# Performance work log

Hardware: AMD Instinct MI355X
Metric: run time of the kernel (lower is better)

## Reference

```python
import jax, jax.numpy as jnp
import numpy as np

DIM = 128
HEADS = 4
WIN = 7
N = WIN * WIN  # 49 tokens per window
B = 64         # images
BDIM = 64      # windows per image (56/7)^2
B_ = B * BDIM  # 4096 total windows
HEAD_DIM = DIM // HEADS
SCALE = HEAD_DIM ** (-0.5)


def _rel_index():
    ch, cw = np.meshgrid(np.arange(WIN), np.arange(WIN), indexing='ij')
    coords = np.stack([ch.ravel(), cw.ravel()])            # [2, N]
    rel = coords[:, :, None] - coords[:, None, :]          # [2, N, N]
    rel = rel.transpose(1, 2, 0).astype(np.int32)
    rel[:, :, 0] += WIN - 1
    rel[:, :, 1] += WIN - 1
    rel[:, :, 0] *= 2 * WIN - 1
    return jnp.asarray(rel.sum(-1))                        # [N, N] in [0, 169)


def setup_inputs() -> dict:
    key = jax.random.key(0)
    ks = jax.random.split(key, 7)
    return {
        'x': jax.random.normal(ks[0], (B_, N, DIM), jnp.float32),
        'q_global': jax.random.normal(ks[1], (B, 1, HEADS, N, HEAD_DIM), jnp.float32),
        'rel_bias_table': jax.random.normal(ks[2], (169, HEADS), jnp.float32) * 0.02,
        'W_kv': jax.random.normal(ks[3], (DIM, 2 * DIM), jnp.float32) / np.sqrt(DIM),
        'b_kv': jnp.zeros((2 * DIM,), jnp.float32),
        'W_proj': jax.random.normal(ks[4], (DIM, DIM), jnp.float32) / np.sqrt(DIM),
        'b_proj': jnp.zeros((DIM,), jnp.float32),
        'rel_index': _rel_index(),
    }


def reference(x, q_global, rel_bias_table, W_kv, b_kv, W_proj, b_proj, rel_index):
    Bw, n, C = x.shape
    Bg = q_global.shape[0]
    bdim = Bw // Bg
    # kv projection: [B_, N, 2, H, hd] -> k, v each [B_, H, N, hd]
    kv = (x @ W_kv + b_kv).reshape(Bw, n, 2, HEADS, HEAD_DIM)
    kv = kv.transpose(2, 0, 3, 1, 4)
    k, v = kv[0], kv[1]
    # broadcast global q over windows of each image
    q = jnp.broadcast_to(q_global, (Bg, bdim, HEADS, n, HEAD_DIM)).reshape(Bw, HEADS, n, HEAD_DIM)
    attn = jnp.einsum('bhnd,bhmd->bhnm', q * SCALE, k)
    bias = rel_bias_table[rel_index]                        # [N, N, H]
    attn = attn + bias.transpose(2, 0, 1)[None]
    attn = jax.nn.softmax(attn, axis=-1)
    out = jnp.einsum('bhnm,bhmd->bhnd', attn, v)
    out = out.transpose(0, 2, 1, 3).reshape(Bw, n, C)
    return out @ W_proj + b_proj
```

## Files before the change

kernel.cpp:

```cpp
#include <hip/hip_runtime.h>

#define SCALE 0.17677669529663687f

typedef __attribute__((ext_vector_type(8))) short bf16x8;
typedef __attribute__((ext_vector_type(4))) short bf16x4;
typedef __attribute__((ext_vector_type(4))) float f32x4;

__device__ inline short cvt_bf16(float f) {
    union { float f; unsigned u; } v; v.f = f;
    unsigned r = v.u + 0x7fffu + ((v.u >> 16) & 1u);
    return (short)(r >> 16);
}
__device__ inline short cvt_bf16_fast(float f) {
    union { float f; unsigned u; } v; v.f = f;
    return (short)((v.u + 0x8000u) >> 16);
}
__device__ inline unsigned pack_bf16x2(float f0, float f1) {
    union { float f; unsigned u; } a, b; a.f = f0; b.f = f1;
    return __builtin_amdgcn_perm(b.u + 0x8000u, a.u + 0x8000u, 0x07060302u);
}

#if __has_builtin(__builtin_amdgcn_mfma_f32_16x16x16bf16_1k)
__device__ inline f32x4 mfma16x16(bf16x4 a, bf16x4 b, f32x4 c) {
    return __builtin_amdgcn_mfma_f32_16x16x16bf16_1k(a, b, c, 0, 0, 0);
}
#else
__device__ inline f32x4 mfma16x16(bf16x4 a, bf16x4 b, f32x4 c) {
    asm("v_mfma_f32_16x16x16_bf16 %0, %1, %2, %0" : "+v"(c) : "v"(a), "v"(b));
    return c;
}
#endif

#define WS_WPT  32768
#define WS_QW   49152
#define WS_BIAS 450560

__global__ void prep_kernel(const float* __restrict__ qg,
                            const float* __restrict__ rbt,
                            const float* __restrict__ wkv,
                            const float* __restrict__ wpj,
                            const int*   __restrict__ ridx,
                            short* __restrict__ ws) {
    int i = blockIdx.x * 256 + threadIdx.x;
    if (i < 32768) {
        int c = i >> 7, k = i & 127;
        ws[i] = cvt_bf16(wkv[k * 256 + c]);
        return;
    }
    i -= 32768;
    if (i < 16384) {
        int c = i >> 7, k = i & 127;
        ws[WS_WPT + i] = cvt_bf16(wpj[k * 128 + c]);
        return;
    }
    i -= 16384;
    if (i < 100352) {
        float4 q4 = *(const float4*)(qg + (long)i * 4);
        unsigned lo = (unsigned)(unsigned short)cvt_bf16(q4.x * SCALE) |
                      ((unsigned)(unsigned short)cvt_bf16(q4.y * SCALE) << 16);
        unsigned hi = (unsigned)(unsigned short)cvt_bf16(q4.z * SCALE) |
                      ((unsigned)(unsigned short)cvt_bf16(q4.w * SCALE) << 16);
        uint2 u; u.x = lo; u.y = hi;
        *(uint2*)(ws + WS_QW + (long)i * 4) = u;
        return;
    }
    i -= 100352;
    if (i < 12544) {
        int h = i / 3136, rem = i % 3136, ir = rem >> 6, j = rem & 63;
        float* bias = (float*)(ws + WS_BIAS);
        bias[i] = (j < 49) ? rbt[ridx[ir * 49 + j] * 4 + h] : 0.f;
    }
}

#define KOFF    6664
#define KSLOT   1960
#define SMEM_SZ 14504

__global__ __launch_bounds__(256, 4) void win_attn_kernel(
        const float* __restrict__ x,
        const short* __restrict__ ws,
        const float* __restrict__ bkv,
        const float* __restrict__ bpj,
        float* __restrict__ out) {
    const int b    = blockIdx.x;
    const int img  = b >> 6;
    const int tid  = threadIdx.x;
    const int w    = tid >> 6;
    const int lane = tid & 63;
    const int quad = lane >> 4;
    const int l16  = lane & 15;

    const short* wkvt  = ws;
    const short* wpt   = ws + WS_WPT;
    const short* qw    = ws + WS_QW;
    const float* biasb = (const float*)(ws + WS_BIAS);

    __shared__ __align__(16) short smem[SMEM_SZ];
    short* xs = smem;
    short* os = smem;

    const f32x4 fzero = {0.f, 0.f, 0.f, 0.f};
    const int h = w;

    const float* xb = x + (long)b * 49 * 128;
    #pragma unroll
    for (int it = 0; it < 4; ++it) {
        int chunk = tid + it * 256;
        if (chunk < 784) {
            int row = chunk >> 4, c8 = (chunk & 15) * 8;
            const float* p = xb + row * 128 + c8;
            float4 a = *(const float4*)p;
            float4 c = *(const float4*)(p + 4);
            union { uint4 u; bf16x8 v; } pk;
            pk.u.x = pack_bf16x2(a.x, a.y);
            pk.u.y = pack_bf16x2(a.z, a.w);
            pk.u.z = pack_bf16x2(c.x, c.y);
            pk.u.w = pack_bf16x2(c.z, c.w);
            *(bf16x8*)(xs + row * 136 + c8) = pk.v;
        }
    }
    __syncthreads();

    short* ksl = smem + KOFF + h * KSLOT;
    {
        f32x4 acck[2][4];
        #pragma unroll
        for (int nt = 0; nt < 2; ++nt)
            #pragma unroll
            for (int mi = 0; mi < 4; ++mi) acck[nt][mi] = fzero;

        #pragma unroll
        for (int kk = 0; kk < 4; ++kk) {
            bf16x8 bfr[2];
            #pragma unroll
            for (int nt = 0; nt < 2; ++nt)
                bfr[nt] = *(const bf16x8*)(wkvt + (h * 32 + nt * 16 + l16) * 128 + kk * 32 + quad * 8);
            #pragma unroll
            for (int mi = 0; mi < 4; ++mi) {
                int tok = mi * 16 + l16; if (tok > 48) tok = 48;
                bf16x8 af = *(const bf16x8*)(xs + tok * 136 + kk * 32 + quad * 8);
                #pragma unroll
                for (int nt = 0; nt < 2; ++nt)
                    acck[nt][mi] = __builtin_amdgcn_mfma_f32_16x16x32_bf16(af, bfr[nt], acck[nt][mi], 0, 0, 0);
            }
        }
        #pragma unroll
        for (int nt = 0; nt < 2; ++nt) {
            const int d = nt * 16 + l16;
            const float bv = bkv[h * 32 + d];
            short* kdst = ksl + d;
            #pragma unroll
            for (int mi = 0; mi < 4; ++mi)
                #pragma unroll
                for (int r = 0; r < 4; ++r) {
                    int tok = mi * 16 + quad * 4 + r;
                    if (tok < 49) kdst[tok * 40] = cvt_bf16_fast(acck[nt][mi][r] + bv);
                }
        }
    }

    bf16x4 vfrag[2][4];
    {
        f32x4 accv[2][4];
        #pragma unroll
        for (int nv = 0; nv < 2; ++nv)
            #pragma unroll
            for (int mi = 0; mi < 4; ++mi) accv[nv][mi] = fzero;

        #pragma unroll
        for (int kk = 0; kk < 4; ++kk) {
            bf16x8 bfr[2];
            #pragma unroll
            for (int nv = 0; nv < 2; ++nv)
                bfr[nv] = *(const bf16x8*)(wkvt + (128 + h * 32 + nv * 16 + l16) * 128 + kk * 32 + quad * 8);
            #pragma unroll
            for (int mi = 0; mi < 4; ++mi) {
                int tok = mi * 16 + l16; if (tok > 48) tok = 48;
                bf16x8 af = *(const bf16x8*)(xs + tok * 136 + kk * 32 + quad * 8);
                #pragma unroll
                for (int nv = 0; nv < 2; ++nv)
                    accv[nv][mi] = __builtin_amdgcn_mfma_f32_16x16x32_bf16(af, bfr[nv], accv[nv][mi], 0, 0, 0);
            }
        }
        #pragma unroll
        for (int nv = 0; nv < 2; ++nv) {
            const float bv = bkv[128 + h * 32 + nv * 16 + l16];
            #pragma unroll
            for (int kt = 0; kt < 4; ++kt) {
                union { unsigned u[2]; bf16x4 v; } pk;
                pk.u[0] = pack_bf16x2(accv[nv][kt][0] + bv, accv[nv][kt][1] + bv);
                pk.u[1] = pack_bf16x2(accv[nv][kt][2] + bv, accv[nv][kt][3] + bv);
                vfrag[nv][kt] = pk.v;
            }
        }
    }

    const short* qh = qw + (long)(img * 4 + h) * 49 * 32;
    f32x4 oacc[4][2];
    #pragma unroll
    for (int mo = 0; mo < 4; ++mo)
        #pragma unroll
        for (int nv = 0; nv < 2; ++nv) oacc[mo][nv] = fzero;

    #pragma unroll
    for (int ni = 0; ni < 4; ++ni) {
        int ic = ni * 16 + l16; if (ic > 48) ic = 48;
        bf16x8 qf = *(const bf16x8*)(qh + ic * 32 + quad * 8);
        f32x4 sacc[4] = {fzero, fzero, fzero, fzero};
        #pragma unroll
        for (int mi = 0; mi < 4; ++mi) {
            int kr = mi * 16 + l16; if (kr > 48) kr = 48;
            bf16x8 kf = *(const bf16x8*)(ksl + kr * 40 + quad * 8);
            sacc[mi] = __builtin_amdgcn_mfma_f32_16x16x32_bf16(kf, qf, sacc[mi], 0, 0, 0);
        }
        const float* bp = biasb + (h * 49 + ic) * 64;
        #pragma unroll
        for (int mi = 0; mi < 4; ++mi) {
            float4 b4 = *(const float4*)(bp + mi * 16 + quad * 4);
            float bb[4] = {b4.x, b4.y, b4.z, b4.w};
            #pragma unroll
            for (int r = 0; r < 4; ++r) {
                int j = mi * 16 + quad * 4 + r;
                sacc[mi][r] = (j < 49) ? (sacc[mi][r] + bb[r]) : -3.0e38f;
            }
        }
        float m = -3.0e38f;
        #pragma unroll
        for (int mi = 0; mi < 4; ++mi)
            #pragma unroll
            for (int r = 0; r < 4; ++r) m = fmaxf(m, sacc[mi][r]);
        m = fmaxf(m, __shfl_xor(m, 16, 64));
        m = fmaxf(m, __shfl_xor(m, 32, 64));
        float sum = 0.f;
        #pragma unroll
        for (int mi = 0; mi < 4; ++mi)
            #pragma unroll
            for (int r = 0; r < 4; ++r) {
                float e = __expf(sacc[mi][r] - m);
                sacc[mi][r] = e; sum += e;
            }
        sum += __shfl_xor(sum, 16, 64);
        sum += __shfl_xor(sum, 32, 64);
        float inv = 1.0f / sum;
        #pragma unroll
        for (int kt = 0; kt < 4; ++kt) {
            union { unsigned u[2]; bf16x4 v; } pk;
            pk.u[0] = pack_bf16x2(sacc[kt][0] * inv, sacc[kt][1] * inv);
            pk.u[1] = pack_bf16x2(sacc[kt][2] * inv, sacc[kt][3] * inv);
            #pragma unroll
            for (int nv = 0; nv < 2; ++nv)
                oacc[ni][nv] = mfma16x16(pk.v, vfrag[nv][kt], oacc[ni][nv]);
        }
    }

    __syncthreads();

    #pragma unroll
    for (int mo = 0; mo < 4; ++mo)
        #pragma unroll
        for (int nv = 0; nv < 2; ++nv)
            #pragma unroll
            for (int r = 0; r < 4; ++r) {
                int tok = mo * 16 + quad * 4 + r;
                os[tok * 136 + h * 32 + nv * 16 + l16] = cvt_bf16_fast(oacc[mo][nv][r]);
            }
    __syncthreads();

    f32x4 pacc[2][4];
    #pragma unroll
    for (int ct = 0; ct < 2; ++ct)
        #pragma unroll
        for (int mi = 0; mi < 4; ++mi) pacc[ct][mi] = fzero;
    #pragma unroll
    for (int kk = 0; kk < 4; ++kk) {
        bf16x8 ofrag[4];
        #pragma unroll
        for (int mi = 0; mi < 4; ++mi)
            ofrag[mi] = *(const bf16x8*)(os + (mi * 16 + l16) * 136 + kk * 32 + quad * 8);
        #pragma unroll
        for (int ct = 0; ct < 2; ++ct) {
            const int c0 = (w * 2 + ct) * 16;
            bf16x8 wfrag = *(const bf16x8*)(wpt + (c0 + l16) * 128 + kk * 32 + quad * 8);
            #pragma unroll
            for (int mi = 0; mi < 4; ++mi)
                pacc[ct][mi] = __builtin_amdgcn_mfma_f32_16x16x32_bf16(ofrag[mi], wfrag, pacc[ct][mi], 0, 0, 0);
        }
    }
    #pragma unroll
    for (int ct = 0; ct < 2; ++ct) {
        const int c0 = (w * 2 + ct) * 16;
        const float bb = bpj[c0 + l16];
        #pragma unroll
        for (int mi = 0; mi < 4; ++mi)
            #pragma unroll
            for (int r = 0; r < 4; ++r) {
                int tok = mi * 16 + quad * 4 + r;
                if (tok < 49)
                    out[((long)b * 49 + tok) * 128 + c0 + l16] = pacc[ct][mi][r] + bb;
            }
    }
}

extern "C" void kernel_launch(void* const* d_in, const int* in_sizes, int n_in,
                              void* d_out, int out_size, void* d_ws, size_t ws_size,
                              hipStream_t stream) {
    const float* x    = (const float*)d_in[0];
    const float* qg   = (const float*)d_in[1];
    const float* rbt  = (const float*)d_in[2];
    const float* wkv  = (const float*)d_in[3];
    const float* bkv  = (const float*)d_in[4];
    const float* wpj  = (const float*)d_in[5];
    const float* bpj  = (const float*)d_in[6];
    const int*   ridx = (const int*)d_in[7];
    short* ws = (short*)d_ws;

    const int prep_total = 32768 + 16384 + 100352 + 12544;
    prep_kernel<<<(prep_total + 255) / 256, 256, 0, stream>>>(qg, rbt, wkv, wpj, ridx, ws);
    win_attn_kernel<<<4096, 256, 0, stream>>>(x, ws, bkv, bpj, (float*)d_out);
}
```

Measured before the change: 270.4 us.

## Load x fragments directly from global into registers, skipping LDS staging

Each wave now loads its x MFMA A-operand fragments straight from global memory into registers, converting to bf16 there, instead of staging the whole tile in LDS and syncing. K slots and the output tile get separate, non-overlapping LDS regions, so one __syncthreads before the output write can be dropped. Output rows are clamped and guarded to 49 tokens. Each of the four waves now reads the full x tile from global (or cache) itself, and the 16 fragment registers held across both projections raise register pressure.

```diff
diff --git a/kernel.cpp b/kernel.cpp
--- a/kernel.cpp
+++ b/kernel.cpp
@@ -72,8 +72,8 @@
     }
 }
 
-#define KOFF    6664
 #define KSLOT   1960
+#define OOFF    7840
 #define SMEM_SZ 14504
 
 __global__ __launch_bounds__(256, 4) void win_attn_kernel(
@@ -96,19 +96,24 @@
     const float* biasb = (const float*)(ws + WS_BIAS);
 
     __shared__ __align__(16) short smem[SMEM_SZ];
-    short* xs = smem;
-    short* os = smem;
+    short* os = smem + OOFF;
 
     const f32x4 fzero = {0.f, 0.f, 0.f, 0.f};
     const int h = w;
 
     const float* xb = x + (long)b * 49 * 128;
-    #pragma unroll
-    for (int it = 0; it < 4; ++it) {
-        int chunk = tid + it * 256;
-        if (chunk < 784) {
-            int row = chunk >> 4, c8 = (chunk & 15) * 8;
-            const float* p = xb + row * 128 + c8;
+    const float* xrow[4];
+    #pragma unroll
+    for (int mi = 0; mi < 4; ++mi) {
+        int tok = mi * 16 + l16; if (tok > 48) tok = 48;
+        xrow[mi] = xb + tok * 128 + quad * 8;
+    }
+    bf16x8 xfrag[4][4];
+    #pragma unroll
+    for (int kk = 0; kk < 4; ++kk)
+        #pragma unroll
+        for (int mi = 0; mi < 4; ++mi) {
+            const float* p = xrow[mi] + kk * 32;
             float4 a = *(const float4*)p;
             float4 c = *(const float4*)(p + 4);
             union { uint4 u; bf16x8 v; } pk;
@@ -116,12 +121,10 @@
             pk.u.y = pack_bf16x2(a.z, a.w);
             pk.u.z = pack_bf16x2(c.x, c.y);
             pk.u.w = pack_bf16x2(c.z, c.w);
-            *(bf16x8*)(xs + row * 136 + c8) = pk.v;
-        }
-    }
-    __syncthreads();
-
-    short* ksl = smem + KOFF + h * KSLOT;
+            xfrag[kk][mi] = pk.v;
+        }
+
+    short* ksl = smem + h * KSLOT;
     {
         f32x4 acck[2][4];
         #pragma unroll
@@ -136,13 +139,10 @@
             for (int nt = 0; nt < 2; ++nt)
                 bfr[nt] = *(const bf16x8*)(wkvt + (h * 32 + nt * 16 + l16) * 128 + kk * 32 + quad * 8);
             #pragma unroll
-            for (int mi = 0; mi < 4; ++mi) {
-                int tok = mi * 16 + l16; if (tok > 48) tok = 48;
-                bf16x8 af = *(const bf16x8*)(xs + tok * 136 + kk * 32 + quad * 8);
+            for (int mi = 0; mi < 4; ++mi)
                 #pragma unroll
                 for (int nt = 0; nt < 2; ++nt)
-                    acck[nt][mi] = __builtin_amdgcn_mfma_f32_16x16x32_bf16(af, bfr[nt], acck[nt][mi], 0, 0, 0);
-            }
+                    acck[nt][mi] = __builtin_amdgcn_mfma_f32_16x16x32_bf16(xfrag[kk][mi], bfr[nt], acck[nt][mi], 0, 0, 0);
         }
         #pragma unroll
         for (int nt = 0; nt < 2; ++nt) {
@@ -174,13 +174,10 @@
             for (int nv = 0; nv < 2; ++nv)
                 bfr[nv] = *(const bf16x8*)(wkvt + (128 + h * 32 + nv * 16 + l16) * 128 + kk * 32 + quad * 8);
             #pragma unroll
-            for (int mi = 0; mi < 4; ++mi) {
-                int tok = mi * 16 + l16; if (tok > 48) tok = 48;
-                bf16x8 af = *(const bf16x8*)(xs + tok * 136 + kk * 32 + quad * 8);
+            for (int mi = 0; mi < 4; ++mi)
                 #pragma unroll
                 for (int nv = 0; nv < 2; ++nv)
-                    accv[nv][mi] = __builtin_amdgcn_mfma_f32_16x16x32_bf16(af, bfr[nv], accv[nv][mi], 0, 0, 0);
-            }
+                    accv[nv][mi] = __builtin_amdgcn_mfma_f32_16x16x32_bf16(xfrag[kk][mi], bfr[nv], accv[nv][mi], 0, 0, 0);
         }
         #pragma unroll
         for (int nv = 0; nv < 2; ++nv) {
@@ -253,8 +250,6 @@
         }
     }
 
-    __syncthreads();
-
     #pragma unroll
     for (int mo = 0; mo < 4; ++mo)
         #pragma unroll
@@ -262,7 +257,8 @@
             #pragma unroll
             for (int r = 0; r < 4; ++r) {
                 int tok = mo * 16 + quad * 4 + r;
-                os[tok * 136 + h * 32 + nv * 16 + l16] = cvt_bf16_fast(oacc[mo][nv][r]);
+                if (tok < 49)
+                    os[tok * 136 + h * 32 + nv * 16 + l16] = cvt_bf16_fast(oacc[mo][nv][r]);
             }
     __syncthreads();
 
@@ -275,8 +271,10 @@
     for (int kk = 0; kk < 4; ++kk) {
         bf16x8 ofrag[4];
         #pragma unroll
-        for (int mi = 0; mi < 4; ++mi)
-            ofrag[mi] = *(const bf16x8*)(os + (mi * 16 + l16) * 136 + kk * 32 + quad * 8);
+        for (int mi = 0; mi < 4; ++mi) {
+            int row = mi * 16 + l16; if (row > 48) row = 48;
+            ofrag[mi] = *(const bf16x8*)(os + row * 136 + kk * 32 + quad * 8);
+        }
         #pragma unroll
         for (int ct = 0; ct < 2; ++ct) {
             const int c0 = (w * 2 + ct) * 16;
```

After: 296.2 us. +9.6%, slower.

## Prefetch weight fragments early, raise MFMA priority, simplify softmax masking

Applied to the files above, without the earlier changes.

The K-projection and output-projection weight fragments, along with the Q and K fragments, are now loaded into registers ahead of the barriers and loops that use them, so their global and LDS latency overlaps with earlier work. MFMA sections are wrapped in s_setprio so matrix work gets issue priority across waves. The padded bias columns are now filled with a large negative value in the prep kernel, which removes the per-element mask compare in the softmax, and the max and sum reductions are rewritten as trees. The prep kernel's transposes now read the source coalesced instead of writing it coalesced. Holding more fragments in registers raises VGPR pressure and could reduce occupancy under launch_bounds(256,4).

```diff
diff --git a/kernel.cpp b/kernel.cpp
--- a/kernel.cpp
+++ b/kernel.cpp
@@ -43,14 +43,14 @@
                             short* __restrict__ ws) {
     int i = blockIdx.x * 256 + threadIdx.x;
     if (i < 32768) {
-        int c = i >> 7, k = i & 127;
-        ws[i] = cvt_bf16(wkv[k * 256 + c]);
+        int k = i >> 8, c = i & 255;
+        ws[c * 128 + k] = cvt_bf16(wkv[i]);
         return;
     }
     i -= 32768;
     if (i < 16384) {
-        int c = i >> 7, k = i & 127;
-        ws[WS_WPT + i] = cvt_bf16(wpj[k * 128 + c]);
+        int k = i >> 7, c = i & 127;
+        ws[WS_WPT + c * 128 + k] = cvt_bf16(wpj[i]);
         return;
     }
     i -= 16384;
@@ -68,7 +68,7 @@
     if (i < 12544) {
         int h = i / 3136, rem = i % 3136, ir = rem >> 6, j = rem & 63;
         float* bias = (float*)(ws + WS_BIAS);
-        bias[i] = (j < 49) ? rbt[ridx[ir * 49 + j] * 4 + h] : 0.f;
+        bias[i] = (j < 49) ? rbt[ridx[ir * 49 + j] * 4 + h] : -3.0e38f;
     }
 }
 
@@ -119,6 +119,12 @@
             *(bf16x8*)(xs + row * 136 + c8) = pk.v;
         }
     }
+    bf16x8 bfrk[4][2];
+    #pragma unroll
+    for (int kk = 0; kk < 4; ++kk)
+        #pragma unroll
+        for (int nt = 0; nt < 2; ++nt)
+            bfrk[kk][nt] = *(const bf16x8*)(wkvt + (h * 32 + nt * 16 + l16) * 128 + kk * 32 + quad * 8);
     __syncthreads();
 
     short* ksl = smem + KOFF + h * KSLOT;
@@ -129,21 +135,19 @@
             #pragma unroll
             for (int mi = 0; mi < 4; ++mi) acck[nt][mi] = fzero;
 
+        __builtin_amdgcn_s_setprio(1);
         #pragma unroll
         for (int kk = 0; kk < 4; ++kk) {
-            bf16x8 bfr[2];
-            #pragma unroll
-            for (int nt = 0; nt < 2; ++nt)
-                bfr[nt] = *(const bf16x8*)(wkvt + (h * 32 + nt * 16 + l16) * 128 + kk * 32 + quad * 8);
             #pragma unroll
             for (int mi = 0; mi < 4; ++mi) {
                 int tok = mi * 16 + l16; if (tok > 48) tok = 48;
                 bf16x8 af = *(const bf16x8*)(xs + tok * 136 + kk * 32 + quad * 8);
                 #pragma unroll
                 for (int nt = 0; nt < 2; ++nt)
-                    acck[nt][mi] = __builtin_amdgcn_mfma_f32_16x16x32_bf16(af, bfr[nt], acck[nt][mi], 0, 0, 0);
-            }
-        }
+                    acck[nt][mi] = __builtin_amdgcn_mfma_f32_16x16x32_bf16(af, bfrk[kk][nt], acck[nt][mi], 0, 0, 0);
+            }
+        }
+        __builtin_amdgcn_s_setprio(0);
         #pragma unroll
         for (int nt = 0; nt < 2; ++nt) {
             const int d = nt * 16 + l16;
@@ -167,6 +171,7 @@
             #pragma unroll
             for (int mi = 0; mi < 4; ++mi) accv[nv][mi] = fzero;
 
+        __builtin_amdgcn_s_setprio(1);
         #pragma unroll
         for (int kk = 0; kk < 4; ++kk) {
             bf16x8 bfr[2];
@@ -182,6 +187,7 @@
                     accv[nv][mi] = __builtin_amdgcn_mfma_f32_16x16x32_bf16(af, bfr[nv], accv[nv][mi], 0, 0, 0);
             }
         }
+        __builtin_amdgcn_s_setprio(0);
         #pragma unroll
         for (int nv = 0; nv < 2; ++nv) {
             const float bv = bkv[128 + h * 32 + nv * 16 + l16];
@@ -196,52 +202,64 @@
     }
 
     const short* qh = qw + (long)(img * 4 + h) * 49 * 32;
-    f32x4 oacc[4][2];
-    #pragma unroll
-    for (int mo = 0; mo < 4; ++mo)
-        #pragma unroll
-        for (int nv = 0; nv < 2; ++nv) oacc[mo][nv] = fzero;
-
+    bf16x8 qfr[4];
     #pragma unroll
     for (int ni = 0; ni < 4; ++ni) {
         int ic = ni * 16 + l16; if (ic > 48) ic = 48;
-        bf16x8 qf = *(const bf16x8*)(qh + ic * 32 + quad * 8);
+        qfr[ni] = *(const bf16x8*)(qh + ic * 32 + quad * 8);
+    }
+    bf16x8 kfr[4];
+    #pragma unroll
+    for (int mi = 0; mi < 4; ++mi) {
+        int kr = mi * 16 + l16; if (kr > 48) kr = 48;
+        kfr[mi] = *(const bf16x8*)(ksl + kr * 40 + quad * 8);
+    }
+
+    f32x4 oacc[4][2];
+    #pragma unroll
+    for (int mo = 0; mo < 4; ++mo)
+        #pragma unroll
+        for (int nv = 0; nv < 2; ++nv) oacc[mo][nv] = fzero;
+
+    #pragma unroll
+    for (int ni = 0; ni < 4; ++ni) {
         f32x4 sacc[4] = {fzero, fzero, fzero, fzero};
-        #pragma unroll
-        for (int mi = 0; mi < 4; ++mi) {
-            int kr = mi * 16 + l16; if (kr > 48) kr = 48;
-            bf16x8 kf = *(const bf16x8*)(ksl + kr * 40 + quad * 8);
-            sacc[mi] = __builtin_amdgcn_mfma_f32_16x16x32_bf16(kf, qf, sacc[mi], 0, 0, 0);
-        }
+        __builtin_amdgcn_s_setprio(1);
+        #pragma unroll
+        for (int mi = 0; mi < 4; ++mi)
+            sacc[mi] = __builtin_amdgcn_mfma_f32_16x16x32_bf16(kfr[mi], qfr[ni], sacc[mi], 0, 0, 0);
+        __builtin_amdgcn_s_setprio(0);
+
+        int ic = ni * 16 + l16; if (ic > 48) ic = 48;
         const float* bp = biasb + (h * 49 + ic) * 64;
         #pragma unroll
         for (int mi = 0; mi < 4; ++mi) {
             float4 b4 = *(const float4*)(bp + mi * 16 + quad * 4);
-            float bb[4] = {b4.x, b4.y, b4.z, b4.w};
-            #pragma unroll
-            for (int r = 0; r < 4; ++r) {
-                int j = mi * 16 + quad * 4 + r;
-                sacc[mi][r] = (j < 49) ? (sacc[mi][r] + bb[r]) : -3.0e38f;
-            }
-        }
-        float m = -3.0e38f;
+            sacc[mi][0] += b4.x; sacc[mi][1] += b4.y;
+            sacc[mi][2] += b4.z; sacc[mi][3] += b4.w;
+        }
+        float mm[4];
         #pragma unroll
         for (int mi = 0; mi < 4; ++mi)
-            #pragma unroll
-            for (int r = 0; r < 4; ++r) m = fmaxf(m, sacc[mi][r]);
+            mm[mi] = fmaxf(fmaxf(fmaxf(sacc[mi][0], sacc[mi][1]), sacc[mi][2]), sacc[mi][3]);
+        float m = fmaxf(fmaxf(mm[0], mm[1]), fmaxf(mm[2], mm[3]));
         m = fmaxf(m, __shfl_xor(m, 16, 64));
         m = fmaxf(m, __shfl_xor(m, 32, 64));
-        float sum = 0.f;
-        #pragma unroll
-        for (int mi = 0; mi < 4; ++mi)
-            #pragma unroll
-            for (int r = 0; r < 4; ++r) {
-                float e = __expf(sacc[mi][r] - m);
-                sacc[mi][r] = e; sum += e;
-            }
+        float ps[4];
+        #pragma unroll
+        for (int mi = 0; mi < 4; ++mi) {
+            float e0 = __expf(sacc[mi][0] - m);
+            float e1 = __expf(sacc[mi][1] - m);
+            float e2 = __expf(sacc[mi][2] - m);
+            float e3 = __expf(sacc[mi][3] - m);
+            sacc[mi][0] = e0; sacc[mi][1] = e1; sacc[mi][2] = e2; sacc[mi][3] = e3;
+            ps[mi] = (e0 + e1) + (e2 + e3);
+        }
+        float sum = (ps[0] + ps[1]) + (ps[2] + ps[3]);
         sum += __shfl_xor(sum, 16, 64);
         sum += __shfl_xor(sum, 32, 64);
         float inv = 1.0f / sum;
+        __builtin_amdgcn_s_setprio(1);
         #pragma unroll
         for (int kt = 0; kt < 4; ++kt) {
             union { unsigned u[2]; bf16x4 v; } pk;
@@ -251,7 +269,15 @@
             for (int nv = 0; nv < 2; ++nv)
                 oacc[ni][nv] = mfma16x16(pk.v, vfrag[nv][kt], oacc[ni][nv]);
         }
-    }
+        __builtin_amdgcn_s_setprio(0);
+    }
+
+    bf16x8 wfragA[4][2];
+    #pragma unroll
+    for (int kk = 0; kk < 4; ++kk)
+        #pragma unroll
+        for (int ct = 0; ct < 2; ++ct)
+            wfragA[kk][ct] = *(const bf16x8*)(wpt + ((w * 2 + ct) * 16 + l16) * 128 + kk * 32 + quad * 8);
 
     __syncthreads();
 
@@ -271,6 +297,7 @@
     for (int ct = 0; ct < 2; ++ct)
         #pragma unroll
         for (int mi = 0; mi < 4; ++mi) pacc[ct][mi] = fzero;
+    __builtin_amdgcn_s_setprio(1);
     #pragma unroll
     for (int kk = 0; kk < 4; ++kk) {
         bf16x8 ofrag[4];
@@ -278,14 +305,12 @@
         for (int mi = 0; mi < 4; ++mi)
             ofrag[mi] = *(const bf16x8*)(os + (mi * 16 + l16) * 136 + kk * 32 + quad * 8);
         #pragma unroll
-        for (int ct = 0; ct < 2; ++ct) {
-            const int c0 = (w * 2 + ct) * 16;
-            bf16x8 wfrag = *(const bf16x8*)(wpt + (c0 + l16) * 128 + kk * 32 + quad * 8);
+        for (int ct = 0; ct < 2; ++ct)
             #pragma unroll
             for (int mi = 0; mi < 4; ++mi)
-                pacc[ct][mi] = __builtin_amdgcn_mfma_f32_16x16x32_bf16(ofrag[mi], wfrag, pacc[ct][mi], 0, 0, 0);
-        }
-    }
+                pacc[ct][mi] = __builtin_amdgcn_mfma_f32_16x16x32_bf16(ofrag[mi], wfragA[kk][ct], pacc[ct][mi], 0, 0, 0);
+    }
+    __builtin_amdgcn_s_setprio(0);
     #pragma unroll
     for (int ct = 0; ct < 2; ++ct) {
         const int c0 = (w * 2 + ct) * 16;
```

New measurement: 267.3 us. Within noise of the previous version (-1.2%).
